# Kernel tuning notes

Measured on AMD Instinct MI355X. Metric: run time of the kernel, lower is better.

The kernel has to match this reference:

```python
import jax, jax.numpy as jnp
import numpy as np

B, N, D, H = 32, 128, 64, 8
DH = D // H  # 8
LN_EPS = 1e-5


def _layer_norm(x, g, b):
    m = jnp.mean(x, axis=-1, keepdims=True)
    v = jnp.mean(jnp.square(x - m), axis=-1, keepdims=True)
    return (x - m) * jax.lax.rsqrt(v + LN_EPS) * g + b


def setup_inputs() -> dict:
    key = jax.random.key(0)
    ks = jax.random.split(key, 16)
    s = 0.05
    return {
        "h": jax.random.normal(ks[0], (B, N, D), jnp.float32),
        "p": jax.random.normal(ks[1], (B, N, D), jnp.float32),
        "e": jax.random.normal(ks[2], (B, N, N, D), jnp.float32),
        "k_RW": jax.random.uniform(ks[3], (B, N, N), jnp.float32),
        # projection weights stored as [in, out] (x @ W == torch Linear)
        "Wq": jax.random.normal(ks[4], (D, D), jnp.float32) * s,
        "Wk": jax.random.normal(ks[5], (D, D), jnp.float32) * s,
        "We": jax.random.normal(ks[6], (D, D), jnp.float32) * s,
        "Wv": jax.random.normal(ks[7], (D, D), jnp.float32) * s,
        "Wo": jax.random.normal(ks[8], (D, D), jnp.float32) * s,
        "bo": jnp.zeros((D,), jnp.float32),
        "ln1_g": jnp.ones((D,), jnp.float32),
        "ln1_b": jnp.zeros((D,), jnp.float32),
        "W1": jax.random.normal(ks[9], (D, 2 * D), jnp.float32) * s,
        "b1": jnp.zeros((2 * D,), jnp.float32),
        "W2": jax.random.normal(ks[10], (2 * D, D), jnp.float32) * s,
        "b2": jnp.zeros((D,), jnp.float32),
        "ln2_g": jnp.ones((D,), jnp.float32),
        "ln2_b": jnp.zeros((D,), jnp.float32),
    }


def reference(h, p, e, k_RW, Wq, Wk, We, Wv, Wo, bo, ln1_g, ln1_b, W1, b1, W2, b2, ln2_g, ln2_b):
    b, n, _ = h.shape
    Qh = (h @ Wq).reshape(b, n, H, DH)
    Kh = (h @ Wk).reshape(b, n, H, DH) * (DH ** -0.5)
    Vh = (h @ Wv).reshape(b, n, H, DH).transpose(0, 2, 1, 3)  # [b,h,n,d]
    E = (e @ We).reshape(b, n, n, H, DH)
    # edge-modulated scores: [b,h,i,j]
    scores = jnp.einsum('bihk,bjhk,bijhk->bhij', Qh, Kh, E)
    scores = jnp.exp(jnp.clip(scores, -5.0, 5.0))
    scores = scores * k_RW[:, None]  # adaptive edge PE scaling
    denom = jnp.maximum(scores.sum(-1, keepdims=True), 1e-6)
    attn = (scores @ Vh) / denom  # [b,h,n,d]
    attn = attn.transpose(0, 2, 1, 3).reshape(b, n, H * DH)
    h1 = h + (attn @ Wo + bo)  # residual + O projection
    h1 = _layer_norm(h1, ln1_g, ln1_b)
    ff = jax.nn.relu(h1 @ W1 + b1) @ W2 + b2
    h2 = _layer_norm(h1 + ff, ln2_g, ln2_b)
    return h2
```

## Files before the change

kernel.cpp:

```cpp
#include <hip/hip_runtime.h>


#define NB 32
#define NN 128
#define ND 64

typedef __attribute__((ext_vector_type(8))) __bf16 bf16x8;
typedef __attribute__((ext_vector_type(8))) unsigned short u16x8;
typedef __attribute__((ext_vector_type(4))) float f32x4;

static __device__ __forceinline__ unsigned short f2bf(float x) {
  unsigned u = __float_as_uint(x);
  u += 0x7fffu + ((u >> 16) & 1u);
  return (unsigned short)(u >> 16);
}

#define DPP_ADD(v, ctrl) \
  ((v) + __int_as_float(__builtin_amdgcn_update_dpp(0, __float_as_int(v), (ctrl), 0xf, 0xf, true)))

static __device__ __forceinline__ float wsum64(float v) {
  v += __shfl_xor(v, 1, 64);
  v += __shfl_xor(v, 2, 64);
  v += __shfl_xor(v, 4, 64);
  v += __shfl_xor(v, 8, 64);
  v += __shfl_xor(v, 16, 64);
  v += __shfl_xor(v, 32, 64);
  return v;
}

static __device__ __forceinline__ float4 xor_add4(float4 a, int m) {
  a.x += __shfl_xor(a.x, m, 64);
  a.y += __shfl_xor(a.y, m, 64);
  a.z += __shfl_xor(a.z, m, 64);
  a.w += __shfl_xor(a.w, m, 64);
  return a;
}

__global__ __launch_bounds__(64) void qkv_kernel(
    const float* __restrict__ h, const float* __restrict__ Wq,
    const float* __restrict__ Wk, const float* __restrict__ Wv,
    const float* __restrict__ We,
    float* __restrict__ Q, float* __restrict__ KT, float* __restrict__ V,
    unsigned short* __restrict__ WeT) {
  if (blockIdx.x == NB * NN) {
    const int t = threadIdx.x;
#pragma unroll
    for (int k0 = 0; k0 < ND; k0 += 8) {
      u16x8 u;
#pragma unroll
      for (int j = 0; j < 8; ++j) u[j] = f2bf(We[(k0 + j) * ND + t]);
      *(u16x8*)(&WeT[t * ND + k0]) = u;
    }
    return;
  }
  const int r = blockIdx.x;
  const int t = threadIdx.x;
  __shared__ float hrow[ND];
  hrow[t] = h[(size_t)r * ND + t];
  __syncthreads();
  float q = 0.f, k = 0.f, v = 0.f;
#pragma unroll 8
  for (int d = 0; d < ND; ++d) {
    const float hv = hrow[d];
    q = fmaf(hv, Wq[d * ND + t], q);
    k = fmaf(hv, Wk[d * ND + t], k);
    v = fmaf(hv, Wv[d * ND + t], v);
  }
  Q[(size_t)r * ND + t] = q;
  KT[((size_t)(r >> 7) * ND + t) * NN + (r & 127)] = k * 0.35355339059327373f;
  V[(size_t)r * ND + t] = v;
}

__global__ __launch_bounds__(64) void fused_kernel(
    const float* __restrict__ h, const float* __restrict__ e,
    const float* __restrict__ kRW,
    const float* __restrict__ Wo, const float* __restrict__ bo,
    const float* __restrict__ g1, const float* __restrict__ be1,
    const float* __restrict__ W1, const float* __restrict__ b1,
    const float* __restrict__ W2, const float* __restrict__ b2,
    const float* __restrict__ g2, const float* __restrict__ be2,
    const float* __restrict__ Q, const float* __restrict__ KT,
    const float* __restrict__ V, const unsigned short* __restrict__ WeT,
    float* __restrict__ out) {
  const int blk = blockIdx.x;
  const int b = blk >> 7;
  const int i = blk & 127;
  const int L = threadIdx.x;
  const int quad = L >> 4;
  const int c4 = L & 15;
  const int lrow = c4;

  __shared__ float S_lds[NN * 9];
  __shared__ float krw_lds[NN];
  __shared__ float q_lds[ND];
  __shared__ float attn_lds[ND];
  __shared__ float n1_lds[ND];
  __shared__ float ff_lds[2 * ND];

  const size_t row = (size_t)b * NN + i;
  const float* e_bi = e + row * (NN * ND);
  const size_t kvbase = (size_t)b * NN * ND;
  const size_t ktbase = (size_t)b * ND * NN;

  q_lds[L] = Q[row * ND + L];
  krw_lds[L] = kRW[row * NN + L];
  krw_lds[64 + L] = kRW[row * NN + 64 + L];

  bf16x8 bfr[2][4];
#pragma unroll
  for (int ks = 0; ks < 2; ++ks)
#pragma unroll
    for (int n0 = 0; n0 < 4; ++n0)
      bfr[ks][n0] = __builtin_bit_cast(
          bf16x8, *(const u16x8*)(&WeT[(n0 * 16 + lrow) * ND + ks * 32 + quad * 8]));

  float4 eb[2][4], ktb[2][4];
#define LD_E(mr, dst)                                              \
  {                                                                \
    const float* p_ = e_bi + ((mr) * 16 + lrow) * ND + quad * 8;   \
    (dst)[0] = *(const float4*)(p_);                               \
    (dst)[1] = *(const float4*)(p_ + 4);                           \
    (dst)[2] = *(const float4*)(p_ + 32);                          \
    (dst)[3] = *(const float4*)(p_ + 36);                          \
  }
#define LD_KT(mr, dst)                                                          \
  {                                                                             \
    _Pragma("unroll")                                                           \
    for (int n0_ = 0; n0_ < 4; ++n0_)                                           \
      (dst)[n0_] = *(const float4*)(&KT[ktbase + (size_t)(n0_ * 16 + lrow) * NN \
                                        + (mr) * 16 + quad * 4]);               \
  }
  LD_E(0, eb[0]); LD_KT(0, ktb[0]);
  LD_E(1, eb[1]); LD_KT(1, ktb[1]);
  __syncthreads();

  float qv[4];
#pragma unroll
  for (int n0 = 0; n0 < 4; ++n0) qv[n0] = q_lds[n0 * 16 + lrow];

#pragma unroll
  for (int mr = 0; mr < 8; ++mr) {
    const int cur = mr & 1;
    bf16x8 afr[2];
#pragma unroll
    for (int ks = 0; ks < 2; ++ks) {
      const float4 v0 = eb[cur][ks * 2], v1 = eb[cur][ks * 2 + 1];
      u16x8 u;
      u[0] = f2bf(v0.x); u[1] = f2bf(v0.y); u[2] = f2bf(v0.z); u[3] = f2bf(v0.w);
      u[4] = f2bf(v1.x); u[5] = f2bf(v1.y); u[6] = f2bf(v1.z); u[7] = f2bf(v1.w);
      afr[ks] = __builtin_bit_cast(bf16x8, u);
    }
    if (mr < 6) LD_E(mr + 2, eb[cur]);

    f32x4 acc[4];
#pragma unroll
    for (int n0 = 0; n0 < 4; ++n0) acc[n0] = (f32x4){0.f, 0.f, 0.f, 0.f};
#pragma unroll
    for (int ks = 0; ks < 2; ++ks)
#pragma unroll
      for (int n0 = 0; n0 < 4; ++n0)
        acc[n0] = __builtin_amdgcn_mfma_f32_16x16x32_bf16(afr[ks], bfr[ks][n0], acc[n0], 0, 0, 0);

    const float4 krw4 = *(const float4*)(&krw_lds[mr * 16 + quad * 4]);
    const float* krwp = (const float*)&krw4;
#pragma unroll
    for (int n0 = 0; n0 < 4; ++n0) {
      const float qn = qv[n0];
      const float* kvp = (const float*)&ktb[cur][n0];
      float sv[4];
#pragma unroll
      for (int reg = 0; reg < 4; ++reg) {
        float tv = acc[n0][reg] * qn * kvp[reg];
        tv = DPP_ADD(tv, 0xB1);
        tv = DPP_ADD(tv, 0x4E);
        tv = DPP_ADD(tv, 0x141);
        sv[reg] = __expf(fminf(fmaxf(tv, -5.f), 5.f)) * krwp[reg];
      }
      if ((L & 7) == 0) {
        const int hh = n0 * 2 + ((L >> 3) & 1);
#pragma unroll
        for (int reg = 0; reg < 4; ++reg)
          S_lds[(mr * 16 + quad * 4 + reg) * 9 + hh] = sv[reg];
      }
    }
    if (mr < 6) LD_KT(mr + 2, ktb[cur]);
  }
  __syncthreads();

  const int jj = L >> 4;
  const int hh2 = c4 >> 1;
  float4 an = make_float4(0.f, 0.f, 0.f, 0.f);
  float den = 0.f;
#pragma unroll 8
  for (int t = 0; t < 32; ++t) {
    const int j = t * 4 + jj;
    const float s = S_lds[j * 9 + hh2];
    const float4 v = *(const float4*)(&V[kvbase + (size_t)j * ND + c4 * 4]);
    an.x = fmaf(s, v.x, an.x);
    an.y = fmaf(s, v.y, an.y);
    an.z = fmaf(s, v.z, an.z);
    an.w = fmaf(s, v.w, an.w);
    den += s;
  }
  an = xor_add4(an, 16); an = xor_add4(an, 32);
  den += __shfl_xor(den, 16, 64); den += __shfl_xor(den, 32, 64);
  const float rden = 1.f / fmaxf(den, 1e-6f);
  if (L < 16)
    *(float4*)(&attn_lds[c4 * 4]) =
        make_float4(an.x * rden, an.y * rden, an.z * rden, an.w * rden);
  __syncthreads();

  float4 o4 = make_float4(0.f, 0.f, 0.f, 0.f);
#pragma unroll 4
  for (int t = 0; t < 16; ++t) {
    const int d = t * 4 + jj;
    const float a = attn_lds[d];
    const float4 wv = *(const float4*)(&Wo[d * ND + c4 * 4]);
    o4.x = fmaf(a, wv.x, o4.x);
    o4.y = fmaf(a, wv.y, o4.y);
    o4.z = fmaf(a, wv.z, o4.z);
    o4.w = fmaf(a, wv.w, o4.w);
  }
  o4 = xor_add4(o4, 16); o4 = xor_add4(o4, 32);
  const float4 bo4 = *(const float4*)(&bo[c4 * 4]);
  const float4 h4 = *(const float4*)(&h[row * ND + c4 * 4]);
  float4 h1;
  h1.x = h4.x + bo4.x + o4.x;
  h1.y = h4.y + bo4.y + o4.y;
  h1.z = h4.z + bo4.z + o4.z;
  h1.w = h4.w + bo4.w + o4.w;
  const float m1 = wsum64(h1.x + h1.y + h1.z + h1.w) * (1.f / 256.f);
  float4 df;
  df.x = h1.x - m1; df.y = h1.y - m1; df.z = h1.z - m1; df.w = h1.w - m1;
  const float v1 =
      wsum64(df.x * df.x + df.y * df.y + df.z * df.z + df.w * df.w) * (1.f / 256.f);
  const float r1 = rsqrtf(v1 + 1e-5f);
  const float4 g14 = *(const float4*)(&g1[c4 * 4]);
  const float4 be14 = *(const float4*)(&be1[c4 * 4]);
  float4 n14;
  n14.x = df.x * r1 * g14.x + be14.x;
  n14.y = df.y * r1 * g14.y + be14.y;
  n14.z = df.z * r1 * g14.z + be14.z;
  n14.w = df.w * r1 * g14.w + be14.w;
  if (L < 16) *(float4*)(&n1_lds[c4 * 4]) = n14;
  __syncthreads();

  const int dd2 = L >> 5;
  const int c5 = L & 31;
  float4 f4 = make_float4(0.f, 0.f, 0.f, 0.f);
#pragma unroll 8
  for (int t = 0; t < 32; ++t) {
    const int d = t * 2 + dd2;
    const float nv = n1_lds[d];
    const float4 wv = *(const float4*)(&W1[d * 128 + c5 * 4]);
    f4.x = fmaf(nv, wv.x, f4.x);
    f4.y = fmaf(nv, wv.y, f4.y);
    f4.z = fmaf(nv, wv.z, f4.z);
    f4.w = fmaf(nv, wv.w, f4.w);
  }
  f4 = xor_add4(f4, 32);
  const float4 b14 = *(const float4*)(&b1[c5 * 4]);
  if (L < 32)
    *(float4*)(&ff_lds[c5 * 4]) =
        make_float4(fmaxf(f4.x + b14.x, 0.f), fmaxf(f4.y + b14.y, 0.f),
                    fmaxf(f4.z + b14.z, 0.f), fmaxf(f4.w + b14.w, 0.f));
  __syncthreads();

  float4 q4 = make_float4(0.f, 0.f, 0.f, 0.f);
#pragma unroll 8
  for (int t = 0; t < 32; ++t) {
    const int u = t * 4 + jj;
    const float fv = ff_lds[u];
    const float4 wv = *(const float4*)(&W2[u * ND + c4 * 4]);
    q4.x = fmaf(fv, wv.x, q4.x);
    q4.y = fmaf(fv, wv.y, q4.y);
    q4.z = fmaf(fv, wv.z, q4.z);
    q4.w = fmaf(fv, wv.w, q4.w);
  }
  q4 = xor_add4(q4, 16); q4 = xor_add4(q4, 32);
  const float4 b24 = *(const float4*)(&b2[c4 * 4]);
  float4 x4;
  x4.x = n14.x + b24.x + q4.x;
  x4.y = n14.y + b24.y + q4.y;
  x4.z = n14.z + b24.z + q4.z;
  x4.w = n14.w + b24.w + q4.w;
  const float m2 = wsum64(x4.x + x4.y + x4.z + x4.w) * (1.f / 256.f);
  float4 d2;
  d2.x = x4.x - m2; d2.y = x4.y - m2; d2.z = x4.z - m2; d2.w = x4.w - m2;
  const float v2 =
      wsum64(d2.x * d2.x + d2.y * d2.y + d2.z * d2.z + d2.w * d2.w) * (1.f / 256.f);
  const float r2 = rsqrtf(v2 + 1e-5f);
  const float4 g24 = *(const float4*)(&g2[c4 * 4]);
  const float4 be24 = *(const float4*)(&be2[c4 * 4]);
  if (L < 16)
    *(float4*)(&out[row * ND + c4 * 4]) =
        make_float4(d2.x * r2 * g24.x + be24.x, d2.y * r2 * g24.y + be24.y,
                    d2.z * r2 * g24.z + be24.z, d2.w * r2 * g24.w + be24.w);
}

extern "C" void kernel_launch(void* const* d_in, const int* in_sizes, int n_in,
                              void* d_out, int out_size, void* d_ws, size_t ws_size,
                              hipStream_t stream) {
  const float* h   = (const float*)d_in[0];
  const float* e   = (const float*)d_in[2];
  const float* kRW = (const float*)d_in[3];
  const float* Wq  = (const float*)d_in[4];
  const float* Wk  = (const float*)d_in[5];
  const float* We  = (const float*)d_in[6];
  const float* Wv  = (const float*)d_in[7];
  const float* Wo  = (const float*)d_in[8];
  const float* bo  = (const float*)d_in[9];
  const float* g1  = (const float*)d_in[10];
  const float* be1 = (const float*)d_in[11];
  const float* W1  = (const float*)d_in[12];
  const float* b1  = (const float*)d_in[13];
  const float* W2  = (const float*)d_in[14];
  const float* b2  = (const float*)d_in[15];
  const float* g2  = (const float*)d_in[16];
  const float* be2 = (const float*)d_in[17];
  float* out = (float*)d_out;

  float* Q  = (float*)d_ws;
  float* KT = Q + (size_t)NB * NN * ND;
  float* V  = KT + (size_t)NB * NN * ND;
  unsigned short* WeT = (unsigned short*)(V + (size_t)NB * NN * ND);

  qkv_kernel<<<NB * NN + 1, 64, 0, stream>>>(h, Wq, Wk, Wv, We, Q, KT, V, WeT);
  fused_kernel<<<NB * NN, 64, 0, stream>>>(h, e, kRW, Wo, bo, g1, be1,
                                           W1, b1, W2, b2, g2, be2, Q, KT, V, WeT, out);
}
```

Baseline: 256.5 us.

## Process four query rows per 256-thread block, staging edges through LDS

Each fused-kernel block now has four waves and handles four query rows i of one batch. Each wave covers two of the eight j-tiles, so the K values a wave needs sit in registers and are reused across all four rows. The e slice for each row is loaded cooperatively, converted to bf16 and staged in LDS with padding before the MFMA. Scores are kept in LDS as bf16, and the per-row epilogue runs one wave per row with wave barriers instead of block barriers. This trades the register double-buffered e prefetch for block-level sync per row, and the bf16 score storage adds rounding error.

```diff
diff --git a/kernel.cpp b/kernel.cpp
--- a/kernel.cpp
+++ b/kernel.cpp
@@ -4,6 +4,7 @@
 #define NB 32
 #define NN 128
 #define ND 64
+#define G 4
 
 typedef __attribute__((ext_vector_type(8))) __bf16 bf16x8;
 typedef __attribute__((ext_vector_type(8))) unsigned short u16x8;
@@ -13,6 +14,9 @@
   unsigned u = __float_as_uint(x);
   u += 0x7fffu + ((u >> 16) & 1u);
   return (unsigned short)(u >> 16);
+}
+static __device__ __forceinline__ float bf2f(unsigned short u) {
+  return __uint_as_float(((unsigned)u) << 16);
 }
 
 #define DPP_ADD(v, ctrl) \
@@ -40,7 +44,7 @@
     const float* __restrict__ h, const float* __restrict__ Wq,
     const float* __restrict__ Wk, const float* __restrict__ Wv,
     const float* __restrict__ We,
-    float* __restrict__ Q, float* __restrict__ KT, float* __restrict__ V,
+    float* __restrict__ Q, float* __restrict__ K, float* __restrict__ V,
     unsigned short* __restrict__ WeT) {
   if (blockIdx.x == NB * NN) {
     const int t = threadIdx.x;
@@ -67,11 +71,11 @@
     v = fmaf(hv, Wv[d * ND + t], v);
   }
   Q[(size_t)r * ND + t] = q;
-  KT[((size_t)(r >> 7) * ND + t) * NN + (r & 127)] = k * 0.35355339059327373f;
+  K[(size_t)r * ND + t] = k * 0.35355339059327373f;
   V[(size_t)r * ND + t] = v;
 }
 
-__global__ __launch_bounds__(64) void fused_kernel(
+__global__ __launch_bounds__(256, 4) void fused_kernel(
     const float* __restrict__ h, const float* __restrict__ e,
     const float* __restrict__ kRW,
     const float* __restrict__ Wo, const float* __restrict__ bo,
@@ -79,32 +83,32 @@
     const float* __restrict__ W1, const float* __restrict__ b1,
     const float* __restrict__ W2, const float* __restrict__ b2,
     const float* __restrict__ g2, const float* __restrict__ be2,
-    const float* __restrict__ Q, const float* __restrict__ KT,
+    const float* __restrict__ Q, const float* __restrict__ K,
     const float* __restrict__ V, const unsigned short* __restrict__ WeT,
     float* __restrict__ out) {
   const int blk = blockIdx.x;
-  const int b = blk >> 7;
-  const int i = blk & 127;
-  const int L = threadIdx.x;
+  const int b = blk >> 5;
+  const int i0 = (blk & 31) * G;
+  const int tid = threadIdx.x;
+  const int w = tid >> 6;
+  const int L = tid & 63;
   const int quad = L >> 4;
-  const int c4 = L & 15;
-  const int lrow = c4;
-
-  __shared__ float S_lds[NN * 9];
-  __shared__ float krw_lds[NN];
-  __shared__ float q_lds[ND];
-  __shared__ float attn_lds[ND];
-  __shared__ float n1_lds[ND];
-  __shared__ float ff_lds[2 * ND];
-
-  const size_t row = (size_t)b * NN + i;
-  const float* e_bi = e + row * (NN * ND);
+  const int lrow = L & 15;
+
+  __shared__ __align__(16) unsigned short e_lds[NN * 72];
+  __shared__ __align__(16) unsigned short S_lds[G * 8 * 136];
+  __shared__ float q_lds[G * ND];
+  __shared__ float krw_lds[G * NN];
+  __shared__ float attn_l[G * ND];
+  __shared__ float n1_l[G * ND];
+  __shared__ float ff_l[G * 2 * ND];
+
+  const size_t row0 = (size_t)b * NN + i0;
   const size_t kvbase = (size_t)b * NN * ND;
-  const size_t ktbase = (size_t)b * ND * NN;
-
-  q_lds[L] = Q[row * ND + L];
-  krw_lds[L] = kRW[row * NN + L];
-  krw_lds[64 + L] = kRW[row * NN + 64 + L];
+
+  q_lds[tid] = Q[row0 * ND + tid];
+  krw_lds[tid] = kRW[row0 * NN + tid];
+  krw_lds[256 + tid] = kRW[row0 * NN + 256 + tid];
 
   bf16x8 bfr[2][4];
 #pragma unroll
@@ -114,87 +118,83 @@
       bfr[ks][n0] = __builtin_bit_cast(
           bf16x8, *(const u16x8*)(&WeT[(n0 * 16 + lrow) * ND + ks * 32 + quad * 8]));
 
-  float4 eb[2][4], ktb[2][4];
-#define LD_E(mr, dst)                                              \
-  {                                                                \
-    const float* p_ = e_bi + ((mr) * 16 + lrow) * ND + quad * 8;   \
-    (dst)[0] = *(const float4*)(p_);                               \
-    (dst)[1] = *(const float4*)(p_ + 4);                           \
-    (dst)[2] = *(const float4*)(p_ + 32);                          \
-    (dst)[3] = *(const float4*)(p_ + 36);                          \
-  }
-#define LD_KT(mr, dst)                                                          \
-  {                                                                             \
-    _Pragma("unroll")                                                           \
-    for (int n0_ = 0; n0_ < 4; ++n0_)                                           \
-      (dst)[n0_] = *(const float4*)(&KT[ktbase + (size_t)(n0_ * 16 + lrow) * NN \
-                                        + (mr) * 16 + quad * 4]);               \
-  }
-  LD_E(0, eb[0]); LD_KT(0, ktb[0]);
-  LD_E(1, eb[1]); LD_KT(1, ktb[1]);
+  float kreg[2][4][4];
+#pragma unroll
+  for (int mt = 0; mt < 2; ++mt)
+#pragma unroll
+    for (int n0 = 0; n0 < 4; ++n0)
+#pragma unroll
+      for (int reg = 0; reg < 4; ++reg)
+        kreg[mt][n0][reg] =
+            K[kvbase + (size_t)((w + mt * 4) * 16 + quad * 4 + reg) * ND + n0 * 16 + lrow];
+
   __syncthreads();
 
-  float qv[4];
-#pragma unroll
-  for (int n0 = 0; n0 < 4; ++n0) qv[n0] = q_lds[n0 * 16 + lrow];
-
-#pragma unroll
-  for (int mr = 0; mr < 8; ++mr) {
-    const int cur = mr & 1;
-    bf16x8 afr[2];
-#pragma unroll
-    for (int ks = 0; ks < 2; ++ks) {
-      const float4 v0 = eb[cur][ks * 2], v1 = eb[cur][ks * 2 + 1];
-      u16x8 u;
-      u[0] = f2bf(v0.x); u[1] = f2bf(v0.y); u[2] = f2bf(v0.z); u[3] = f2bf(v0.w);
-      u[4] = f2bf(v1.x); u[5] = f2bf(v1.y); u[6] = f2bf(v1.z); u[7] = f2bf(v1.w);
-      afr[ks] = __builtin_bit_cast(bf16x8, u);
+  for (int g = 0; g < G; ++g) {
+    const float* ep = e + (row0 + g) * (size_t)(NN * ND);
+#pragma unroll
+    for (int p = 0; p < 8; ++p) {
+      const int idx = p * 1024 + tid * 4;
+      const float4 v = *(const float4*)(ep + idx);
+      const int r = idx >> 6;
+      const int c = idx & 63;
+      *(ushort4*)(&e_lds[r * 72 + c]) =
+          make_ushort4(f2bf(v.x), f2bf(v.y), f2bf(v.z), f2bf(v.w));
     }
-    if (mr < 6) LD_E(mr + 2, eb[cur]);
-
-    f32x4 acc[4];
-#pragma unroll
-    for (int n0 = 0; n0 < 4; ++n0) acc[n0] = (f32x4){0.f, 0.f, 0.f, 0.f};
-#pragma unroll
-    for (int ks = 0; ks < 2; ++ks)
-#pragma unroll
-      for (int n0 = 0; n0 < 4; ++n0)
-        acc[n0] = __builtin_amdgcn_mfma_f32_16x16x32_bf16(afr[ks], bfr[ks][n0], acc[n0], 0, 0, 0);
-
-    const float4 krw4 = *(const float4*)(&krw_lds[mr * 16 + quad * 4]);
-    const float* krwp = (const float*)&krw4;
-#pragma unroll
-    for (int n0 = 0; n0 < 4; ++n0) {
-      const float qn = qv[n0];
-      const float* kvp = (const float*)&ktb[cur][n0];
-      float sv[4];
-#pragma unroll
-      for (int reg = 0; reg < 4; ++reg) {
-        float tv = acc[n0][reg] * qn * kvp[reg];
-        tv = DPP_ADD(tv, 0xB1);
-        tv = DPP_ADD(tv, 0x4E);
-        tv = DPP_ADD(tv, 0x141);
-        sv[reg] = __expf(fminf(fmaxf(tv, -5.f), 5.f)) * krwp[reg];
-      }
-      if ((L & 7) == 0) {
-        const int hh = n0 * 2 + ((L >> 3) & 1);
-#pragma unroll
-        for (int reg = 0; reg < 4; ++reg)
-          S_lds[(mr * 16 + quad * 4 + reg) * 9 + hh] = sv[reg];
+    __syncthreads();
+#pragma unroll
+    for (int mt = 0; mt < 2; ++mt) {
+      const int mr = w + mt * 4;
+      bf16x8 afr[2];
+#pragma unroll
+      for (int ks = 0; ks < 2; ++ks)
+        afr[ks] = __builtin_bit_cast(
+            bf16x8, *(const u16x8*)(&e_lds[(mr * 16 + lrow) * 72 + ks * 32 + quad * 8]));
+      f32x4 acc[4];
+#pragma unroll
+      for (int n0 = 0; n0 < 4; ++n0) acc[n0] = (f32x4){0.f, 0.f, 0.f, 0.f};
+#pragma unroll
+      for (int ks = 0; ks < 2; ++ks)
+#pragma unroll
+        for (int n0 = 0; n0 < 4; ++n0)
+          acc[n0] =
+              __builtin_amdgcn_mfma_f32_16x16x32_bf16(afr[ks], bfr[ks][n0], acc[n0], 0, 0, 0);
+
+      const float4 krw4 = *(const float4*)(&krw_lds[g * NN + mr * 16 + quad * 4]);
+      const float* krwp = (const float*)&krw4;
+#pragma unroll
+      for (int n0 = 0; n0 < 4; ++n0) {
+        const float qn = q_lds[g * ND + n0 * 16 + lrow];
+        float sv[4];
+#pragma unroll
+        for (int reg = 0; reg < 4; ++reg) {
+          float tv = acc[n0][reg] * qn * kreg[mt][n0][reg];
+          tv = DPP_ADD(tv, 0xB1);
+          tv = DPP_ADD(tv, 0x4E);
+          tv = DPP_ADD(tv, 0x141);
+          sv[reg] = __expf(fminf(fmaxf(tv, -5.f), 5.f)) * krwp[reg];
+        }
+        if ((L & 7) == 0) {
+          const int hh = n0 * 2 + ((L >> 3) & 1);
+          *(ushort4*)(&S_lds[(g * 8 + hh) * 136 + mr * 16 + quad * 4]) =
+              make_ushort4(f2bf(sv[0]), f2bf(sv[1]), f2bf(sv[2]), f2bf(sv[3]));
+        }
       }
     }
-    if (mr < 6) LD_KT(mr + 2, ktb[cur]);
-  }
-  __syncthreads();
-
+    __syncthreads();
+  }
+
+  const size_t row = row0 + w;
   const int jj = L >> 4;
+  const int c4 = L & 15;
   const int hh2 = c4 >> 1;
+
   float4 an = make_float4(0.f, 0.f, 0.f, 0.f);
   float den = 0.f;
 #pragma unroll 8
   for (int t = 0; t < 32; ++t) {
     const int j = t * 4 + jj;
-    const float s = S_lds[j * 9 + hh2];
+    const float s = bf2f(S_lds[(w * 8 + hh2) * 136 + j]);
     const float4 v = *(const float4*)(&V[kvbase + (size_t)j * ND + c4 * 4]);
     an.x = fmaf(s, v.x, an.x);
     an.y = fmaf(s, v.y, an.y);
@@ -206,15 +206,15 @@
   den += __shfl_xor(den, 16, 64); den += __shfl_xor(den, 32, 64);
   const float rden = 1.f / fmaxf(den, 1e-6f);
   if (L < 16)
-    *(float4*)(&attn_lds[c4 * 4]) =
+    *(float4*)(&attn_l[w * ND + c4 * 4]) =
         make_float4(an.x * rden, an.y * rden, an.z * rden, an.w * rden);
-  __syncthreads();
+  __builtin_amdgcn_wave_barrier();
 
   float4 o4 = make_float4(0.f, 0.f, 0.f, 0.f);
 #pragma unroll 4
   for (int t = 0; t < 16; ++t) {
     const int d = t * 4 + jj;
-    const float a = attn_lds[d];
+    const float a = attn_l[w * ND + d];
     const float4 wv = *(const float4*)(&Wo[d * ND + c4 * 4]);
     o4.x = fmaf(a, wv.x, o4.x);
     o4.y = fmaf(a, wv.y, o4.y);
@@ -242,8 +242,8 @@
   n14.y = df.y * r1 * g14.y + be14.y;
   n14.z = df.z * r1 * g14.z + be14.z;
   n14.w = df.w * r1 * g14.w + be14.w;
-  if (L < 16) *(float4*)(&n1_lds[c4 * 4]) = n14;
-  __syncthreads();
+  if (L < 16) *(float4*)(&n1_l[w * ND + c4 * 4]) = n14;
+  __builtin_amdgcn_wave_barrier();
 
   const int dd2 = L >> 5;
   const int c5 = L & 31;
@@ -251,7 +251,7 @@
 #pragma unroll 8
   for (int t = 0; t < 32; ++t) {
     const int d = t * 2 + dd2;
-    const float nv = n1_lds[d];
+    const float nv = n1_l[w * ND + d];
     const float4 wv = *(const float4*)(&W1[d * 128 + c5 * 4]);
     f4.x = fmaf(nv, wv.x, f4.x);
     f4.y = fmaf(nv, wv.y, f4.y);
@@ -261,16 +261,16 @@
   f4 = xor_add4(f4, 32);
   const float4 b14 = *(const float4*)(&b1[c5 * 4]);
   if (L < 32)
-    *(float4*)(&ff_lds[c5 * 4]) =
+    *(float4*)(&ff_l[w * 2 * ND + c5 * 4]) =
         make_float4(fmaxf(f4.x + b14.x, 0.f), fmaxf(f4.y + b14.y, 0.f),
                     fmaxf(f4.z + b14.z, 0.f), fmaxf(f4.w + b14.w, 0.f));
-  __syncthreads();
+  __builtin_amdgcn_wave_barrier();
 
   float4 q4 = make_float4(0.f, 0.f, 0.f, 0.f);
 #pragma unroll 8
   for (int t = 0; t < 32; ++t) {
     const int u = t * 4 + jj;
-    const float fv = ff_lds[u];
+    const float fv = ff_l[w * 2 * ND + u];
     const float4 wv = *(const float4*)(&W2[u * ND + c4 * 4]);
     q4.x = fmaf(fv, wv.x, q4.x);
     q4.y = fmaf(fv, wv.y, q4.y);
@@ -320,12 +320,12 @@
   const float* be2 = (const float*)d_in[17];
   float* out = (float*)d_out;
 
-  float* Q  = (float*)d_ws;
-  float* KT = Q + (size_t)NB * NN * ND;
-  float* V  = KT + (size_t)NB * NN * ND;
+  float* Q = (float*)d_ws;
+  float* K = Q + (size_t)NB * NN * ND;
+  float* V = K + (size_t)NB * NN * ND;
   unsigned short* WeT = (unsigned short*)(V + (size_t)NB * NN * ND);
 
-  qkv_kernel<<<NB * NN + 1, 64, 0, stream>>>(h, Wq, Wk, Wv, We, Q, KT, V, WeT);
-  fused_kernel<<<NB * NN, 64, 0, stream>>>(h, e, kRW, Wo, bo, g1, be1,
-                                           W1, b1, W2, b2, g2, be2, Q, KT, V, WeT, out);
-}
+  qkv_kernel<<<NB * NN + 1, 64, 0, stream>>>(h, Wq, Wk, Wv, We, Q, K, V, WeT);
+  fused_kernel<<<NB * NN / G, 256, 0, stream>>>(h, e, kRW, Wo, bo, g1, be1,
+                                                W1, b1, W2, b2, g2, be2, Q, K, V, WeT, out);
+}
```

Result: faster. 249.6 us (-2.7%).
